# Kernel tuning notes

Hardware: AMD Instinct MI355X
Metric: run time of the kernel (lower is better)

The kernel has to match this reference:

```python
import jax, jax.numpy as jnp
import numpy as np

B, S, D, H = 2, 2048, 512, 8
DK = D // H
DECAY = 0.02
LN_EPS = 1e-5


def setup_inputs() -> dict:
    key = jax.random.key(0)
    ks = jax.random.split(key, 16)
    sd = 1.0 / np.sqrt(D)
    def lin(k, fan_in, fan_out):
        return jax.random.uniform(k, (fan_in, fan_out), jnp.float32, -sd, sd)
    return {
        "x": jax.random.normal(ks[0], (B, S, D), jnp.float32),
        "wq": lin(ks[1], D, D), "bq": jnp.zeros((D,), jnp.float32),
        "wk": lin(ks[2], D, D), "bk": jnp.zeros((D,), jnp.float32),
        "wv": lin(ks[3], D, D), "bv": jnp.zeros((D,), jnp.float32),
        "wo": lin(ks[4], D, D), "bo": jnp.zeros((D,), jnp.float32),
        "g1_w": lin(ks[5], D, D // 2), "g1_b": jnp.zeros((D // 2,), jnp.float32),
        "g2_w": lin(ks[6], D // 2, 1), "g2_b": jnp.zeros((1,), jnp.float32),
        "ln_g": jnp.ones((D,), jnp.float32), "ln_b": jnp.zeros((D,), jnp.float32),
    }


def _temporal_bias(seq_len):
    # exp(-decay * |i-j|) masked to lower triangle (causal), additive bias
    pos = jnp.arange(seq_len)
    dist = jnp.abs(pos[:, None] - pos[None, :]).astype(jnp.float32)
    bias = jnp.exp(-DECAY * dist)
    return jnp.tril(bias)  # (S, S)


def reference(x, wq, bq, wk, bk, wv, bv, wo, bo, g1_w, g1_b, g2_w, g2_b, ln_g, ln_b):
    b, s, d = x.shape
    # projections -> (B, H, S, DK)
    q = (x @ wq + bq).reshape(b, s, H, DK).transpose(0, 2, 1, 3)
    k = (x @ wk + bk).reshape(b, s, H, DK).transpose(0, 2, 1, 3)
    v = (x @ wv + bv).reshape(b, s, H, DK).transpose(0, 2, 1, 3)
    scores = jnp.einsum("bhqd,bhkd->bhqk", q, k) / jnp.sqrt(jnp.float32(DK))
    scores = scores + _temporal_bias(s)[None, None, :, :]
    attn = jax.nn.softmax(scores, axis=-1)  # (B, H, S, S)
    out = jnp.einsum("bhqk,bhkd->bhqd", attn, v)
    out = out.transpose(0, 2, 1, 3).reshape(b, s, d)
    out = out @ wo + bo
    # gated residual
    gate = jax.nn.sigmoid(jax.nn.relu(x @ g1_w + g1_b) @ g2_w + g2_b)  # (B, S, 1)
    out = out * gate + x * (1.0 - gate)
    # layer norm
    mu = jnp.mean(out, axis=-1, keepdims=True)
    var = jnp.var(out, axis=-1, keepdims=True)
    y = (out - mu) / jnp.sqrt(var + LN_EPS) * ln_g + ln_b
    return (y, attn)
```

## Files before the change

kernel.cpp:

```cpp
#include <hip/hip_runtime.h>

#define BB 2
#define SS 2048
#define DD 512
#define HH 8
#define DKK 64
#define NROWS (BB * SS)
#define Y_SIZE (BB * SS * DD)

typedef __attribute__((ext_vector_type(8))) short short8;
typedef __attribute__((ext_vector_type(4))) float f32x4;

__device__ __forceinline__ ushort f2bf(float f) {
  union { float f; unsigned u; } v; v.f = f;
  unsigned u = v.u;
  return (ushort)((u + 0x7fffu + ((u >> 16) & 1u)) >> 16);
}


__global__ __launch_bounds__(256) void conv_x_kernel(const float* __restrict__ x,
                                                     ushort* __restrict__ xb) {
  int i = (blockIdx.x * 256 + threadIdx.x) * 4;
  float4 v = *(const float4*)(x + i);
  ushort4 o = {f2bf(v.x), f2bf(v.y), f2bf(v.z), f2bf(v.w)};
  *(ushort4*)(xb + i) = o;
}

__global__ __launch_bounds__(256) void conv_wt_kernel(
    const float* __restrict__ w0, const float* __restrict__ w1,
    const float* __restrict__ w2, const float* __restrict__ w3,
    ushort* __restrict__ o0, ushort* __restrict__ o1,
    ushort* __restrict__ o2, ushort* __restrict__ o3) {
  __shared__ float T[64][65];
  const float* w; ushort* wt;
  switch (blockIdx.z) {
    case 0: w = w0; wt = o0; break;
    case 1: w = w1; wt = o1; break;
    case 2: w = w2; wt = o2; break;
    default: w = w3; wt = o3; break;
  }
  const int t = threadIdx.x;
  const int n0 = blockIdx.x * 64, k0 = blockIdx.y * 64;
#pragma unroll
  for (int i = 0; i < 4; ++i) {
    int c = t + i * 256;
    int row = c >> 4, cc = c & 15;
    float4 v = *(const float4*)(w + (size_t)(k0 + row) * DD + n0 + cc * 4);
    T[row][cc * 4 + 0] = v.x; T[row][cc * 4 + 1] = v.y;
    T[row][cc * 4 + 2] = v.z; T[row][cc * 4 + 3] = v.w;
  }
  __syncthreads();
#pragma unroll
  for (int i = 0; i < 2; ++i) {
    int c = t + i * 256;
    int nr = c >> 3, kc = c & 7;
    ushort4 a, b;
    a.x = f2bf(T[kc * 8 + 0][nr]); a.y = f2bf(T[kc * 8 + 1][nr]);
    a.z = f2bf(T[kc * 8 + 2][nr]); a.w = f2bf(T[kc * 8 + 3][nr]);
    b.x = f2bf(T[kc * 8 + 4][nr]); b.y = f2bf(T[kc * 8 + 5][nr]);
    b.z = f2bf(T[kc * 8 + 6][nr]); b.w = f2bf(T[kc * 8 + 7][nr]);
    *(ushort4*)(wt + (size_t)(n0 + nr) * DD + k0 + kc * 8) = a;
    *(ushort4*)(wt + (size_t)(n0 + nr) * DD + k0 + kc * 8 + 4) = b;
  }
}


__device__ __forceinline__ void mfma_gemm64(
    const ushort* __restrict__ A, int lda, const ushort* __restrict__ B, int ldb,
    int K, ushort (*As)[72], ushort (*Bs)[72], f32x4 (&acc)[2][2], int t) {
  const int l = t & 63, w = t >> 6;
  const int mq = w & 1, nq = w >> 1;
  const int l15 = l & 15, l4 = l >> 4;
  for (int k0 = 0; k0 < K; k0 += 64) {
    __syncthreads();
#pragma unroll
    for (int i = 0; i < 2; ++i) {
      int c = t + i * 256;
      int row = c >> 3, cc = c & 7;
      *(uint4*)&As[row][cc * 8] = *(const uint4*)(A + (size_t)row * lda + k0 + cc * 8);
      *(uint4*)&Bs[row][cc * 8] = *(const uint4*)(B + (size_t)row * ldb + k0 + cc * 8);
    }
    __syncthreads();
    short8 af[2][2], bf[2][2];
#pragma unroll
    for (int mt = 0; mt < 2; ++mt)
#pragma unroll
      for (int ks = 0; ks < 2; ++ks)
        af[mt][ks] = *(const short8*)&As[32 * mq + 16 * mt + l15][ks * 32 + l4 * 8];
#pragma unroll
    for (int nt = 0; nt < 2; ++nt)
#pragma unroll
      for (int ks = 0; ks < 2; ++ks)
        bf[nt][ks] = *(const short8*)&Bs[32 * nq + 16 * nt + l15][ks * 32 + l4 * 8];
#pragma unroll
    for (int mt = 0; mt < 2; ++mt)
#pragma unroll
      for (int nt = 0; nt < 2; ++nt)
#pragma unroll
        for (int ks = 0; ks < 2; ++ks)
          acc[mt][nt] = __builtin_amdgcn_mfma_f32_16x16x32_bf16(
              af[mt][ks], bf[nt][ks], acc[mt][nt], 0, 0, 0);
  }
}


__global__ __launch_bounds__(256) void proj_qkv_kernel(
    const ushort* __restrict__ xb,
    const ushort* __restrict__ wqt, const float* __restrict__ bq,
    const ushort* __restrict__ wkt, const float* __restrict__ bk,
    const ushort* __restrict__ wvt, const float* __restrict__ bv,
    ushort* __restrict__ qb, ushort* __restrict__ kb, ushort* __restrict__ vt) {
  __shared__ ushort As[64][72], Bs[64][72];
  const ushort* W; const float* bias; ushort* out;
  if (blockIdx.z == 0) { W = wqt; bias = bq; out = qb; }
  else if (blockIdx.z == 1) { W = wkt; bias = bk; out = kb; }
  else { W = wvt; bias = bv; out = vt; }
  const float scale = (blockIdx.z == 0) ? 0.125f : 1.0f;
  const int m0 = blockIdx.x * 64;
  const int h = blockIdx.y;
  const int t = threadIdx.x;
  const int l = t & 63, w = t >> 6;
  const int mq = w & 1, nq = w >> 1;
  const int l15 = l & 15, l4 = l >> 4;
  f32x4 acc[2][2] = {};
  mfma_gemm64(xb + (size_t)m0 * DD, DD, W + (size_t)h * DKK * DD, DD, DD,
              As, Bs, acc, t);
  float biasv[2];
#pragma unroll
  for (int nt = 0; nt < 2; ++nt) biasv[nt] = bias[h * DKK + 32 * nq + 16 * nt + l15];

  if (blockIdx.z < 2) {
    __syncthreads();
#pragma unroll
    for (int mt = 0; mt < 2; ++mt)
#pragma unroll
      for (int nt = 0; nt < 2; ++nt)
#pragma unroll
        for (int r = 0; r < 4; ++r)
          As[32 * mq + 16 * mt + l4 * 4 + r][32 * nq + 16 * nt + l15] =
              f2bf((acc[mt][nt][r] + biasv[nt]) * scale);
    __syncthreads();
#pragma unroll
    for (int i = 0; i < 2; ++i) {
      int c = t + i * 256;
      int row = c >> 3, cc = c & 7;
      int m = m0 + row, b = m >> 11, s = m & (SS - 1);
      uint4 v = *(const uint4*)&As[row][cc * 8];
      *(uint4*)(out + ((size_t)(b * HH + h) * SS + s) * DKK + cc * 8) = v;
    }
  } else {
#pragma unroll
    for (int mt = 0; mt < 2; ++mt)
#pragma unroll
      for (int nt = 0; nt < 2; ++nt) {
        int dk = 32 * nq + 16 * nt + l15;
        int m = m0 + 32 * mq + 16 * mt + l4 * 4;
        int b = m >> 11, sb = m & (SS - 1);
        ushort4 pk;
        pk.x = f2bf(acc[mt][nt][0] + biasv[nt]);
        pk.y = f2bf(acc[mt][nt][1] + biasv[nt]);
        pk.z = f2bf(acc[mt][nt][2] + biasv[nt]);
        pk.w = f2bf(acc[mt][nt][3] + biasv[nt]);
        *(ushort4*)(out + ((size_t)(b * HH + h) * DKK + dk) * SS + sb) = pk;
      }
  }
}


__global__ __launch_bounds__(256) void attn_kernel(
    const ushort* __restrict__ qb, const ushort* __restrict__ kb,
    const ushort* __restrict__ vt, float* __restrict__ attn,
    ushort* __restrict__ ctx) {
  __shared__ ushort Ks[64][72], Vs[64][72], Ps[64][72];
  __shared__ float rs[64];
  const int t = threadIdx.x;
  const int l = t & 63, w = t >> 6;
  const int mq = w & 1, nq = w >> 1;
  const int l15 = l & 15, l4 = l >> 4;
  const int z = blockIdx.y;
  const int q0 = blockIdx.x * 64;
  if (t < 64) rs[t] = 0.f;

  short8 qf[2][2];
#pragma unroll
  for (int bt = 0; bt < 2; ++bt)
#pragma unroll
    for (int ks = 0; ks < 2; ++ks)
      qf[bt][ks] = *(const short8*)(qb +
          ((size_t)z * SS + q0 + 32 * mq + 16 * bt + l15) * DKK + ks * 32 + l4 * 8);

  int qi_[2]; float rowf[2];
#pragma unroll
  for (int bt = 0; bt < 2; ++bt) {
    qi_[bt] = q0 + 32 * mq + 16 * bt + l15;
    rowf[bt] = __expf(-0.02f * (float)qi_[bt]);
  }
  const float c_r[4] = {1.0f, 1.0202013f, 1.0408108f, 1.0618365f};

  float rsp[2] = {0.f, 0.f};
  f32x4 oacc[2][2] = {};

  for (int kt = 0; kt < 32; ++kt) {
    __syncthreads();
#pragma unroll
    for (int i = 0; i < 2; ++i) {
      int c = t + i * 256;
      int row = c >> 3, cc = c & 7;
      *(uint4*)&Ks[row][cc * 8] =
          *(const uint4*)(kb + ((size_t)z * SS + kt * 64 + row) * DKK + cc * 8);
      *(uint4*)&Vs[row][cc * 8] =
          *(const uint4*)(vt + ((size_t)z * DKK + row) * SS + kt * 64 + cc * 8);
    }
    __syncthreads();
    short8 kf[2][2];
#pragma unroll
    for (int at = 0; at < 2; ++at)
#pragma unroll
      for (int ks = 0; ks < 2; ++ks)
        kf[at][ks] = *(const short8*)&Ks[32 * nq + 16 * at + l15][ks * 32 + l4 * 8];
    f32x4 acc[2][2] = {};
#pragma unroll
    for (int at = 0; at < 2; ++at)
#pragma unroll
      for (int bt = 0; bt < 2; ++bt)
#pragma unroll
        for (int ks = 0; ks < 2; ++ks)
          acc[at][bt] = __builtin_amdgcn_mfma_f32_16x16x32_bf16(
              kf[at][ks], qf[bt][ks], acc[at][bt], 0, 0, 0);
#pragma unroll
    for (int at = 0; at < 2; ++at) {
      const int kjbase = kt * 64 + 32 * nq + 16 * at + l4 * 4;
      const float colb = __expf(0.02f * (float)kjbase);
#pragma unroll
      for (int bt = 0; bt < 2; ++bt) {
        const float rc = rowf[bt] * colb;
        ushort4 us;
        float pv[4];
#pragma unroll
        for (int r = 0; r < 4; ++r) {
          float bias = (kjbase + r <= qi_[bt]) ? rc * c_r[r] : 0.f;
          float p = __expf(acc[at][bt][r] + bias);
          pv[r] = p;
          rsp[bt] += p;
        }
        us.x = f2bf(pv[0]); us.y = f2bf(pv[1]);
        us.z = f2bf(pv[2]); us.w = f2bf(pv[3]);
        *(ushort4*)&Ps[32 * mq + 16 * bt + l15][32 * nq + 16 * at + l4 * 4] = us;
      }
    }
    __syncthreads();
    short8 pa[2][2], pb[2][2];
#pragma unroll
    for (int mt = 0; mt < 2; ++mt)
#pragma unroll
      for (int ks = 0; ks < 2; ++ks)
        pa[mt][ks] = *(const short8*)&Ps[32 * mq + 16 * mt + l15][ks * 32 + l4 * 8];
#pragma unroll
    for (int nt = 0; nt < 2; ++nt)
#pragma unroll
      for (int ks = 0; ks < 2; ++ks)
        pb[nt][ks] = *(const short8*)&Vs[32 * nq + 16 * nt + l15][ks * 32 + l4 * 8];
#pragma unroll
    for (int mt = 0; mt < 2; ++mt)
#pragma unroll
      for (int nt = 0; nt < 2; ++nt)
#pragma unroll
        for (int ks = 0; ks < 2; ++ks)
          oacc[mt][nt] = __builtin_amdgcn_mfma_f32_16x16x32_bf16(
              pa[mt][ks], pb[nt][ks], oacc[mt][nt], 0, 0, 0);
  }

#pragma unroll
  for (int bt = 0; bt < 2; ++bt) {
    float v = rsp[bt];
    v += __shfl_xor(v, 16);
    v += __shfl_xor(v, 32);
    if (l < 16) atomicAdd(&rs[32 * mq + 16 * bt + l], v);
  }
  __syncthreads();
  float invr[2][4], rowf2[2][4]; int qi2_[2][4];
#pragma unroll
  for (int mt = 0; mt < 2; ++mt)
#pragma unroll
    for (int r = 0; r < 4; ++r) {
      int qi2 = q0 + 32 * mq + 16 * mt + l4 * 4 + r;
      qi2_[mt][r] = qi2;
      rowf2[mt][r] = __expf(-0.02f * (float)qi2);
      invr[mt][r] = 1.f / rs[32 * mq + 16 * mt + l4 * 4 + r];
    }

#pragma unroll
  for (int mt = 0; mt < 2; ++mt)
#pragma unroll
    for (int nt = 0; nt < 2; ++nt)
#pragma unroll
      for (int r = 0; r < 4; ++r)
        Ps[32 * mq + 16 * mt + l4 * 4 + r][32 * nq + 16 * nt + l15] =
            f2bf(oacc[mt][nt][r] * invr[mt][r]);
  __syncthreads();
  {
    const int b = z >> 3, h = z & 7;
#pragma unroll
    for (int i = 0; i < 2; ++i) {
      int c = t + i * 256;
      int row = c >> 3, cc = c & 7;
      uint4 v = *(const uint4*)&Ps[row][cc * 8];
      *(uint4*)(ctx + ((size_t)(b * SS + q0 + row)) * DD + h * DKK + cc * 8) = v;
    }
  }

  const int srow = t >> 3, scol = (t & 7) * 8;
  const int srow2 = srow + 32;
  __syncthreads();
  {
    const ushort* p = kb + (size_t)z * SS * DKK;
    *(uint4*)&Ks[srow][scol]  = *(const uint4*)(p + (size_t)srow * DKK + scol);
    *(uint4*)&Ks[srow2][scol] = *(const uint4*)(p + (size_t)srow2 * DKK + scol);
  }
  __syncthreads();
  for (int kt = 0; kt < 32; ++kt) {
    ushort (*cur)[72] = (kt & 1) ? Vs : Ks;
    ushort (*nxt)[72] = (kt & 1) ? Ks : Vs;
    uint4 s0, s1;
    if (kt < 31) {
      const ushort* p = kb + ((size_t)z * SS + (kt + 1) * 64) * DKK;
      s0 = *(const uint4*)(p + (size_t)srow * DKK + scol);
      s1 = *(const uint4*)(p + (size_t)srow2 * DKK + scol);
    }
    short8 kf[2][2];
#pragma unroll
    for (int nt = 0; nt < 2; ++nt)
#pragma unroll
      for (int ks = 0; ks < 2; ++ks)
        kf[nt][ks] = *(const short8*)&cur[32 * nq + 16 * nt + l15][ks * 32 + l4 * 8];
    f32x4 acc[2][2] = {};
#pragma unroll
    for (int mt = 0; mt < 2; ++mt)
#pragma unroll
      for (int nt = 0; nt < 2; ++nt)
#pragma unroll
        for (int ks = 0; ks < 2; ++ks)
          acc[mt][nt] = __builtin_amdgcn_mfma_f32_16x16x32_bf16(
              qf[mt][ks], kf[nt][ks], acc[mt][nt], 0, 0, 0);
#pragma unroll
    for (int nt = 0; nt < 2; ++nt) {
      const int kj = kt * 64 + 32 * nq + 16 * nt + l15;
      const float colf = __expf(0.02f * (float)kj);
#pragma unroll
      for (int mt = 0; mt < 2; ++mt) {
        const size_t rbase = ((size_t)z * SS + qi2_[mt][0]) * SS + kj;
#pragma unroll
        for (int r = 0; r < 4; ++r) {
          float bias = (kj <= qi2_[mt][r]) ? rowf2[mt][r] * colf : 0.f;
          float p = __expf(acc[mt][nt][r] + bias) * invr[mt][r];
          attn[rbase + (size_t)r * SS] = p;
        }
      }
    }
    if (kt < 31) {
      *(uint4*)&nxt[srow][scol]  = s0;
      *(uint4*)&nxt[srow2][scol] = s1;
    }
    __syncthreads();
  }
}


__global__ __launch_bounds__(256) void proj_o_kernel(
    const ushort* __restrict__ ctx, const ushort* __restrict__ wot,
    const float* __restrict__ bo, float* __restrict__ o) {
  __shared__ ushort As[64][72], Bs[64][72];
  const int m0 = blockIdx.x * 64, n0 = blockIdx.y * 64;
  const int t = threadIdx.x;
  const int l = t & 63, w = t >> 6;
  const int mq = w & 1, nq = w >> 1;
  const int l15 = l & 15, l4 = l >> 4;
  f32x4 acc[2][2] = {};
  mfma_gemm64(ctx + (size_t)m0 * DD, DD, wot + (size_t)n0 * DD, DD, DD,
              As, Bs, acc, t);
#pragma unroll
  for (int nt = 0; nt < 2; ++nt) {
    int col = n0 + 32 * nq + 16 * nt + l15;
    float bv = bo[col];
#pragma unroll
    for (int mt = 0; mt < 2; ++mt)
#pragma unroll
      for (int r = 0; r < 4; ++r) {
        int m = m0 + 32 * mq + 16 * mt + l4 * 4 + r;
        o[(size_t)m * DD + col] = acc[mt][nt][r] + bv;
      }
  }
}


__global__ __launch_bounds__(256) void gate_kernel(
    const float* __restrict__ x, const float* __restrict__ g1w,
    const float* __restrict__ g1b, const float* __restrict__ g2w,
    const float* __restrict__ g2b, float* __restrict__ gate) {
  __shared__ float xs[8][512];
  __shared__ float red[32];
  const int r0 = blockIdx.x * 8;
  const int t = threadIdx.x;
  const float4* xg = (const float4*)&x[(size_t)r0 * DD];
  float4* xsv = (float4*)&xs[0][0];
#pragma unroll
  for (int i = 0; i < 4; ++i) xsv[t + i * 256] = xg[t + i * 256];
  __syncthreads();
  float acc[8] = {};
  for (int i = 0; i < 512; i += 4) {
    float w0 = g1w[(i + 0) * 256 + t];
    float w1 = g1w[(i + 1) * 256 + t];
    float w2 = g1w[(i + 2) * 256 + t];
    float w3 = g1w[(i + 3) * 256 + t];
#pragma unroll
    for (int r = 0; r < 8; ++r) {
      float4 xv = *(const float4*)&xs[r][i];
      acc[r] += xv.x * w0 + xv.y * w1 + xv.z * w2 + xv.w * w3;
    }
  }
  float b1 = g1b[t], w2_ = g2w[t];
  float p[8];
#pragma unroll
  for (int r = 0; r < 8; ++r) {
    float h = acc[r] + b1;
    h = h > 0.f ? h : 0.f;
    p[r] = h * w2_;
  }
#pragma unroll
  for (int r = 0; r < 8; ++r)
    for (int off = 32; off; off >>= 1) p[r] += __shfl_xor(p[r], off, 64);
  if ((t & 63) == 0) {
#pragma unroll
    for (int r = 0; r < 8; ++r) red[r * 4 + (t >> 6)] = p[r];
  }
  __syncthreads();
  if (t < 8) {
    float s = red[t * 4] + red[t * 4 + 1] + red[t * 4 + 2] + red[t * 4 + 3] + g2b[0];
    gate[r0 + t] = 1.f / (1.f + __expf(-s));
  }
}


__global__ __launch_bounds__(256) void blend_ln_kernel(
    const float* __restrict__ o, const float* __restrict__ x,
    const float* __restrict__ gate, const float* __restrict__ ln_g,
    const float* __restrict__ ln_b, float* __restrict__ y) {
  __shared__ float r1[4], r2[4];
  const int row = blockIdx.x, t = threadIdx.x;
  float g = gate[row];
  float2 o2 = *(const float2*)&o[(size_t)row * DD + t * 2];
  float2 x2 = *(const float2*)&x[(size_t)row * DD + t * 2];
  float va = o2.x * g + x2.x * (1.f - g);
  float vb = o2.y * g + x2.y * (1.f - g);
  float s = va + vb, q = va * va + vb * vb;
  for (int off = 32; off; off >>= 1) {
    s += __shfl_xor(s, off, 64);
    q += __shfl_xor(q, off, 64);
  }
  if ((t & 63) == 0) { r1[t >> 6] = s; r2[t >> 6] = q; }
  __syncthreads();
  s = r1[0] + r1[1] + r1[2] + r1[3];
  q = r2[0] + r2[1] + r2[2] + r2[3];
  float mean = s * (1.f / 512.f);
  float var = q * (1.f / 512.f) - mean * mean;
  float rstd = rsqrtf(var + 1e-5f);
  float2 lg = *(const float2*)&ln_g[t * 2];
  float2 lb = *(const float2*)&ln_b[t * 2];
  float2 out;
  out.x = (va - mean) * rstd * lg.x + lb.x;
  out.y = (vb - mean) * rstd * lg.y + lb.y;
  *(float2*)&y[(size_t)row * DD + t * 2] = out;
}

extern "C" void kernel_launch(void* const* d_in, const int* in_sizes, int n_in,
                              void* d_out, int out_size, void* d_ws, size_t ws_size,
                              hipStream_t stream) {
  const float* x   = (const float*)d_in[0];
  const float* wq  = (const float*)d_in[1];
  const float* bq  = (const float*)d_in[2];
  const float* wk  = (const float*)d_in[3];
  const float* bk  = (const float*)d_in[4];
  const float* wv  = (const float*)d_in[5];
  const float* bv  = (const float*)d_in[6];
  const float* wo  = (const float*)d_in[7];
  const float* bo  = (const float*)d_in[8];
  const float* g1w = (const float*)d_in[9];
  const float* g1b = (const float*)d_in[10];
  const float* g2w = (const float*)d_in[11];
  const float* g2b = (const float*)d_in[12];
  const float* lng = (const float*)d_in[13];
  const float* lnb = (const float*)d_in[14];

  float* y    = (float*)d_out;
  float* attn = y + (size_t)Y_SIZE;

  char* ws = (char*)d_ws;
  ushort* xb  = (ushort*)(ws);
  ushort* wqt = (ushort*)(ws + (4 << 20));
  ushort* wkt = (ushort*)(ws + (4 << 20) + (512 << 10));
  ushort* wvt = (ushort*)(ws + (5 << 20));
  ushort* wot = (ushort*)(ws + (5 << 20) + (512 << 10));
  ushort* qb  = (ushort*)(ws + (6 << 20));
  ushort* kb  = (ushort*)(ws + (10 << 20));
  ushort* vt  = (ushort*)(ws + (14 << 20));
  ushort* ctx = (ushort*)(ws + (18 << 20));
  float*  o   = (float*)(ws + (22 << 20));
  float*  gate= (float*)(ws + (30 << 20));

  hipLaunchKernelGGL(conv_x_kernel, dim3(Y_SIZE / 1024), dim3(256), 0, stream, x, xb);
  hipLaunchKernelGGL(conv_wt_kernel, dim3(8, 8, 4), dim3(256), 0, stream,
                     wq, wk, wv, wo, wqt, wkt, wvt, wot);
  hipLaunchKernelGGL(proj_qkv_kernel, dim3(64, 8, 3), dim3(256), 0, stream,
                     xb, wqt, bq, wkt, bk, wvt, bv, qb, kb, vt);
  hipLaunchKernelGGL(gate_kernel, dim3(512), dim3(256), 0, stream,
                     x, g1w, g1b, g2w, g2b, gate);
  hipLaunchKernelGGL(attn_kernel, dim3(32, 16), dim3(256), 0, stream,
                     qb, kb, vt, attn, ctx);
  hipLaunchKernelGGL(proj_o_kernel, dim3(64, 8), dim3(256), 0, stream,
                     ctx, wot, bo, o);
  hipLaunchKernelGGL(blend_ln_kernel, dim3(4096), dim3(256), 0, stream,
                     o, x, gate, lng, lnb, y);
}
```

Measured before the change: 458.2 us.

## Halve attention query tile to 32 rows and use exp2 with folded log2e

The attention kernel now handles 32 query rows per block instead of 64, doubling the grid to 1024 blocks, and each wave owns a 16-key column slice. The aim is better occupancy and load balance across the CUs (launch bounds ask for 4 blocks per CU). Separately, log2(e) is folded into the Q scale and the bias row factor so exp2f can replace __expf. The cost is that each block now reloads the full K and V for only half as many queries, doubling K/V traffic per query.

Measured after the change: 426.5 us. 1.07x faster.

```diff
diff --git a/kernel.cpp b/kernel.cpp
--- a/kernel.cpp
+++ b/kernel.cpp
@@ -115,7 +115,7 @@
   if (blockIdx.z == 0) { W = wqt; bias = bq; out = qb; }
   else if (blockIdx.z == 1) { W = wkt; bias = bk; out = kb; }
   else { W = wvt; bias = bv; out = vt; }
-  const float scale = (blockIdx.z == 0) ? 0.125f : 1.0f;
+  const float scale = (blockIdx.z == 0) ? 0.1803368801f : 1.0f;
   const int m0 = blockIdx.x * 64;
   const int h = blockIdx.y;
   const int t = threadIdx.x;
@@ -167,19 +167,18 @@
 }
 
 
-__global__ __launch_bounds__(256) void attn_kernel(
+__global__ __launch_bounds__(256, 4) void attn_kernel(
     const ushort* __restrict__ qb, const ushort* __restrict__ kb,
     const ushort* __restrict__ vt, float* __restrict__ attn,
     ushort* __restrict__ ctx) {
-  __shared__ ushort Ks[64][72], Vs[64][72], Ps[64][72];
-  __shared__ float rs[64];
+  __shared__ ushort Ks[64][72], Vs[64][72], Ps[32][72];
+  __shared__ float rs[32];
   const int t = threadIdx.x;
-  const int l = t & 63, w = t >> 6;
-  const int mq = w & 1, nq = w >> 1;
+  const int l = t & 63, nq = t >> 6;
   const int l15 = l & 15, l4 = l >> 4;
   const int z = blockIdx.y;
-  const int q0 = blockIdx.x * 64;
-  if (t < 64) rs[t] = 0.f;
+  const int q0 = blockIdx.x * 32;
+  if (t < 32) rs[t] = 0.f;
 
   short8 qf[2][2];
 #pragma unroll
@@ -187,18 +186,19 @@
 #pragma unroll
     for (int ks = 0; ks < 2; ++ks)
       qf[bt][ks] = *(const short8*)(qb +
-          ((size_t)z * SS + q0 + 32 * mq + 16 * bt + l15) * DKK + ks * 32 + l4 * 8);
-
+          ((size_t)z * SS + q0 + 16 * bt + l15) * DKK + ks * 32 + l4 * 8);
+
+  const float LOG2E = 1.4426950409f;
   int qi_[2]; float rowf[2];
 #pragma unroll
   for (int bt = 0; bt < 2; ++bt) {
-    qi_[bt] = q0 + 32 * mq + 16 * bt + l15;
-    rowf[bt] = __expf(-0.02f * (float)qi_[bt]);
+    qi_[bt] = q0 + 16 * bt + l15;
+    rowf[bt] = LOG2E * __expf(-0.02f * (float)qi_[bt]);
   }
   const float c_r[4] = {1.0f, 1.0202013f, 1.0408108f, 1.0618365f};
 
   float rsp[2] = {0.f, 0.f};
-  f32x4 oacc[2][2] = {};
+  f32x4 oacc[2] = {};
 
   for (int kt = 0; kt < 32; ++kt) {
     __syncthreads();
@@ -212,24 +212,19 @@
           *(const uint4*)(vt + ((size_t)z * DKK + row) * SS + kt * 64 + cc * 8);
     }
     __syncthreads();
-    short8 kf[2][2];
-#pragma unroll
-    for (int at = 0; at < 2; ++at)
+    short8 kf[2];
+#pragma unroll
+    for (int ks = 0; ks < 2; ++ks)
+      kf[ks] = *(const short8*)&Ks[16 * nq + l15][ks * 32 + l4 * 8];
+    f32x4 acc[2] = {};
+#pragma unroll
+    for (int bt = 0; bt < 2; ++bt)
 #pragma unroll
       for (int ks = 0; ks < 2; ++ks)
-        kf[at][ks] = *(const short8*)&Ks[32 * nq + 16 * at + l15][ks * 32 + l4 * 8];
-    f32x4 acc[2][2] = {};
-#pragma unroll
-    for (int at = 0; at < 2; ++at)
-#pragma unroll
-      for (int bt = 0; bt < 2; ++bt)
-#pragma unroll
-        for (int ks = 0; ks < 2; ++ks)
-          acc[at][bt] = __builtin_amdgcn_mfma_f32_16x16x32_bf16(
-              kf[at][ks], qf[bt][ks], acc[at][bt], 0, 0, 0);
-#pragma unroll
-    for (int at = 0; at < 2; ++at) {
-      const int kjbase = kt * 64 + 32 * nq + 16 * at + l4 * 4;
+        acc[bt] = __builtin_amdgcn_mfma_f32_16x16x32_bf16(
+            kf[ks], qf[bt][ks], acc[bt], 0, 0, 0);
+    {
+      const int kjbase = kt * 64 + 16 * nq + l4 * 4;
       const float colb = __expf(0.02f * (float)kjbase);
 #pragma unroll
       for (int bt = 0; bt < 2; ++bt) {
@@ -239,35 +234,31 @@
 #pragma unroll
         for (int r = 0; r < 4; ++r) {
           float bias = (kjbase + r <= qi_[bt]) ? rc * c_r[r] : 0.f;
-          float p = __expf(acc[at][bt][r] + bias);
+          float p = exp2f(acc[bt][r] + bias);
           pv[r] = p;
           rsp[bt] += p;
         }
         us.x = f2bf(pv[0]); us.y = f2bf(pv[1]);
         us.z = f2bf(pv[2]); us.w = f2bf(pv[3]);
-        *(ushort4*)&Ps[32 * mq + 16 * bt + l15][32 * nq + 16 * at + l4 * 4] = us;
+        *(ushort4*)&Ps[16 * bt + l15][16 * nq + l4 * 4] = us;
       }
     }
     __syncthreads();
-    short8 pa[2][2], pb[2][2];
+    short8 pa[2][2], pb[2];
 #pragma unroll
     for (int mt = 0; mt < 2; ++mt)
 #pragma unroll
       for (int ks = 0; ks < 2; ++ks)
-        pa[mt][ks] = *(const short8*)&Ps[32 * mq + 16 * mt + l15][ks * 32 + l4 * 8];
-#pragma unroll
-    for (int nt = 0; nt < 2; ++nt)
+        pa[mt][ks] = *(const short8*)&Ps[16 * mt + l15][ks * 32 + l4 * 8];
+#pragma unroll
+    for (int ks = 0; ks < 2; ++ks)
+      pb[ks] = *(const short8*)&Vs[16 * nq + l15][ks * 32 + l4 * 8];
+#pragma unroll
+    for (int mt = 0; mt < 2; ++mt)
 #pragma unroll
       for (int ks = 0; ks < 2; ++ks)
-        pb[nt][ks] = *(const short8*)&Vs[32 * nq + 16 * nt + l15][ks * 32 + l4 * 8];
-#pragma unroll
-    for (int mt = 0; mt < 2; ++mt)
-#pragma unroll
-      for (int nt = 0; nt < 2; ++nt)
-#pragma unroll
-        for (int ks = 0; ks < 2; ++ks)
-          oacc[mt][nt] = __builtin_amdgcn_mfma_f32_16x16x32_bf16(
-              pa[mt][ks], pb[nt][ks], oacc[mt][nt], 0, 0, 0);
+        oacc[mt] = __builtin_amdgcn_mfma_f32_16x16x32_bf16(
+            pa[mt][ks], pb[ks], oacc[mt], 0, 0, 0);
   }
 
 #pragma unroll
@@ -275,7 +266,7 @@
     float v = rsp[bt];
     v += __shfl_xor(v, 16);
     v += __shfl_xor(v, 32);
-    if (l < 16) atomicAdd(&rs[32 * mq + 16 * bt + l], v);
+    if (l < 16) atomicAdd(&rs[16 * bt + l], v);
   }
   __syncthreads();
   float invr[2][4], rowf2[2][4]; int qi2_[2][4];
@@ -283,30 +274,23 @@
   for (int mt = 0; mt < 2; ++mt)
 #pragma unroll
     for (int r = 0; r < 4; ++r) {
-      int qi2 = q0 + 32 * mq + 16 * mt + l4 * 4 + r;
+      int qi2 = q0 + 16 * mt + l4 * 4 + r;
       qi2_[mt][r] = qi2;
-      rowf2[mt][r] = __expf(-0.02f * (float)qi2);
-      invr[mt][r] = 1.f / rs[32 * mq + 16 * mt + l4 * 4 + r];
+      rowf2[mt][r] = LOG2E * __expf(-0.02f * (float)qi2);
+      invr[mt][r] = 1.f / rs[16 * mt + l4 * 4 + r];
     }
 
 #pragma unroll
   for (int mt = 0; mt < 2; ++mt)
 #pragma unroll
-    for (int nt = 0; nt < 2; ++nt)
-#pragma unroll
-      for (int r = 0; r < 4; ++r)
-        Ps[32 * mq + 16 * mt + l4 * 4 + r][32 * nq + 16 * nt + l15] =
-            f2bf(oacc[mt][nt][r] * invr[mt][r]);
+    for (int r = 0; r < 4; ++r)
+      Ps[16 * mt + l4 * 4 + r][16 * nq + l15] = f2bf(oacc[mt][r] * invr[mt][r]);
   __syncthreads();
   {
     const int b = z >> 3, h = z & 7;
-#pragma unroll
-    for (int i = 0; i < 2; ++i) {
-      int c = t + i * 256;
-      int row = c >> 3, cc = c & 7;
-      uint4 v = *(const uint4*)&Ps[row][cc * 8];
-      *(uint4*)(ctx + ((size_t)(b * SS + q0 + row)) * DD + h * DKK + cc * 8) = v;
-    }
+    const int row = t >> 3, cc = t & 7;
+    *(uint4*)(ctx + ((size_t)(b * SS + q0 + row)) * DD + h * DKK + cc * 8) =
+        *(const uint4*)&Ps[row][cc * 8];
   }
 
   const int srow = t >> 3, scol = (t & 7) * 8;
@@ -327,24 +311,19 @@
       s0 = *(const uint4*)(p + (size_t)srow * DKK + scol);
       s1 = *(const uint4*)(p + (size_t)srow2 * DKK + scol);
     }
-    short8 kf[2][2];
-#pragma unroll
-    for (int nt = 0; nt < 2; ++nt)
+    short8 kf[2];
+#pragma unroll
+    for (int ks = 0; ks < 2; ++ks)
+      kf[ks] = *(const short8*)&cur[16 * nq + l15][ks * 32 + l4 * 8];
+    f32x4 acc[2] = {};
+#pragma unroll
+    for (int mt = 0; mt < 2; ++mt)
 #pragma unroll
       for (int ks = 0; ks < 2; ++ks)
-        kf[nt][ks] = *(const short8*)&cur[32 * nq + 16 * nt + l15][ks * 32 + l4 * 8];
-    f32x4 acc[2][2] = {};
-#pragma unroll
-    for (int mt = 0; mt < 2; ++mt)
-#pragma unroll
-      for (int nt = 0; nt < 2; ++nt)
-#pragma unroll
-        for (int ks = 0; ks < 2; ++ks)
-          acc[mt][nt] = __builtin_amdgcn_mfma_f32_16x16x32_bf16(
-              qf[mt][ks], kf[nt][ks], acc[mt][nt], 0, 0, 0);
-#pragma unroll
-    for (int nt = 0; nt < 2; ++nt) {
-      const int kj = kt * 64 + 32 * nq + 16 * nt + l15;
+        acc[mt] = __builtin_amdgcn_mfma_f32_16x16x32_bf16(
+            qf[mt][ks], kf[ks], acc[mt], 0, 0, 0);
+    {
+      const int kj = kt * 64 + 16 * nq + l15;
       const float colf = __expf(0.02f * (float)kj);
 #pragma unroll
       for (int mt = 0; mt < 2; ++mt) {
@@ -352,7 +331,7 @@
 #pragma unroll
         for (int r = 0; r < 4; ++r) {
           float bias = (kj <= qi2_[mt][r]) ? rowf2[mt][r] * colf : 0.f;
-          float p = __expf(acc[mt][nt][r] + bias) * invr[mt][r];
+          float p = exp2f(acc[mt][r] + bias) * invr[mt][r];
           attn[rbase + (size_t)r * SS] = p;
         }
       }
@@ -514,7 +493,7 @@
                      xb, wqt, bq, wkt, bk, wvt, bv, qb, kb, vt);
   hipLaunchKernelGGL(gate_kernel, dim3(512), dim3(256), 0, stream,
                      x, g1w, g1b, g2w, g2b, gate);
-  hipLaunchKernelGGL(attn_kernel, dim3(32, 16), dim3(256), 0, stream,
+  hipLaunchKernelGGL(attn_kernel, dim3(64, 16), dim3(256), 0, stream,
                      qb, kb, vt, attn, ctx);
   hipLaunchKernelGGL(proj_o_kernel, dim3(64, 8), dim3(256), 0, stream,
                      ctx, wot, bo, o);
```
